# Kernel tuning notes

Measured on AMD Instinct MI355X. Metric: run time of the kernel, lower is better.

The kernel has to match this reference:

```python
import jax, jax.numpy as jnp
import numpy as np

BS, C, D = 4096, 16384, 128
POS_ALPHA, POS_DELTA = 32.0, 0.1
NEG_ALPHA, NEG_DELTA = 32.0, -0.1


def _normalize(x):
    # F.normalize(x, dim=1)
    return x / jnp.linalg.norm(x, axis=1, keepdims=True)


def _masked_lse(sims, mask, axis, use_max):
    """Faithful port of Criterion.masked_logsumexp (returns per-entry lse and the
    nonzero-entry mask that torch uses to filter before the final mean)."""
    m = sims * mask
    if use_max:
        ref = jnp.max(m, axis=axis, keepdims=True)
    else:
        ref = jnp.min(m, axis=axis, keepdims=True)
    ref = jax.lax.stop_gradient(ref)  # torch: ref_v.detach()
    # torch: nz_entries = max + min of (sims*mask); keep where nonzero
    nz = (jnp.max(m, axis=axis) + jnp.min(m, axis=axis)) != 0
    s = jnp.sum(jnp.exp(sims - ref) * mask, axis=axis)
    lse = jnp.log(jnp.where(nz, s, 1.0)) + jnp.squeeze(ref, axis=axis)
    return lse, nz


def setup_inputs() -> dict:
    key = jax.random.key(0)
    k1, k2, k3 = jax.random.split(key, 3)
    batch = jax.random.normal(k1, (BS, D), dtype=jnp.float32)
    # proxies = randn/proxy_div, init_dev=0 so no max-shift
    proxies = jax.random.normal(k2, (C, D), dtype=jnp.float32) / 8.0
    labels = jax.random.randint(k3, (BS,), 0, C)
    return {"batch": batch, "proxies": proxies, "labels": labels}


def reference(batch, proxies, labels):
    batch = _normalize(batch)          # [BS, D]
    proxies = _normalize(proxies)      # [C, D]

    pos_sims = batch @ proxies[labels].T   # [BS, BS] cosine sims to positive proxies
    sims = batch @ proxies.T               # [BS, C]

    same = (labels[:, None] == labels[None, :]).astype(batch.dtype)              # [BS, BS]
    diff = (labels[:, None] != jnp.arange(C)[None, :]).astype(batch.dtype)       # [BS, C]

    w_pos = -POS_ALPHA * (pos_sims - POS_DELTA)
    w_neg = NEG_ALPHA * (sims - NEG_DELTA)

    # mode='anchor' -> dim=0; cosine -> max=False for pos, max=True for neg
    pos_lse, pos_nz = _masked_lse(w_pos, same, axis=0, use_max=False)
    neg_lse, neg_nz = _masked_lse(w_neg, diff, axis=0, use_max=True)

    # nca_clean=False -> softplus
    pos_s = jax.nn.softplus(pos_lse)
    neg_s = jax.nn.softplus(neg_lse)

    # torch takes mean only over nz entries
    pos_mean = jnp.sum(jnp.where(pos_nz, pos_s, 0.0)) / jnp.maximum(jnp.sum(pos_nz), 1).astype(batch.dtype)
    neg_mean = jnp.sum(jnp.where(neg_nz, neg_s, 0.0)) / jnp.maximum(jnp.sum(neg_nz), 1).astype(batch.dtype)
    return pos_mean + neg_mean
```

## Files before the change

kernel.cpp:

```cpp
#include <hip/hip_runtime.h>
#include <math.h>

#define BS 4096
#define C_CLS 16384
#define D 128
#define NS 16
#define NR 4
#define KE 46.16624130844683f
#define POS_C 4.616624130844683f
#define LN2 0.69314718055994531f
#define CORR_BLOCKS 256
#define NEG_BLOCKS 2048

typedef __attribute__((ext_vector_type(8))) short short8;
typedef __attribute__((ext_vector_type(4))) float f32x4;

__device__ inline float bf2f(unsigned short h) {
    return __uint_as_float(((unsigned)h) << 16);
}
__device__ inline unsigned short f2bf(float f) {
    unsigned u = __float_as_uint(f);
    u += 0x7FFF + ((u >> 16) & 1);
    return (unsigned short)(u >> 16);
}
__device__ inline float fastexp2(float x) {
    return __int_as_float((int)fmaf(x, 8388608.0f, 1064866816.0f));
}
__device__ inline float softplus(float x) {
    return fmaxf(x, 0.0f) + log1pf(__expf(-fabsf(x)));
}
__device__ inline void gload16(const void* g, void* l) {
    __builtin_amdgcn_global_load_lds((const __attribute__((address_space(1))) void*)g,
                                     (__attribute__((address_space(3))) void*)l, 16, 0, 0);
}
__device__ inline unsigned fenc(float f) {
    unsigned u = __float_as_uint(f);
    return (u & 0x80000000u) ? ~u : (u | 0x80000000u);
}
__device__ inline float fdec(unsigned k) {
    return (k & 0x80000000u) ? __uint_as_float(k ^ 0x80000000u) : __uint_as_float(~k);
}

__global__ __launch_bounds__(256) void normalize_all(const float* __restrict__ batch,
                                                     const float* __restrict__ proxies,
                                                     short* __restrict__ bbf,
                                                     short* __restrict__ pbf,
                                                     float* __restrict__ acc,
                                                     float* __restrict__ negSub,
                                                     float* __restrict__ posSum,
                                                     float* __restrict__ posCnt,
                                                     unsigned* __restrict__ posMaxK,
                                                     unsigned* __restrict__ posMinK,
                                                     int* __restrict__ counter) {
    const int sub = threadIdx.x >> 5;
    const int lane32 = threadIdx.x & 31;
    const int row = blockIdx.x * 8 + sub;
    const bool isb = row < BS;
    const float* src = isb ? batch : proxies;
    short* dst = isb ? bbf : pbf;
    const int r = isb ? row : row - BS;
    const float sc = isb ? 1.0f : KE;

    float4 v = ((const float4*)(src + (size_t)r * D))[lane32];
    float ss = v.x * v.x + v.y * v.y + v.z * v.z + v.w * v.w;
#pragma unroll
    for (int off = 16; off; off >>= 1) ss += __shfl_xor(ss, off);
    float inv = rsqrtf(ss) * sc;
    ushort4 o;
    o.x = f2bf(v.x * inv);
    o.y = f2bf(v.y * inv);
    o.z = f2bf(v.z * inv);
    o.w = f2bf(v.w * inv);
    ((ushort4*)(dst + (size_t)r * D))[lane32] = o;

    const int bid = blockIdx.x, t = threadIdx.x;
    if (bid < 64) negSub[bid * 256 + t] = 0.0f;
    else if (bid < 128) posSum[(bid - 64) * 256 + t] = 0.0f;
    else if (bid < 192) posCnt[(bid - 128) * 256 + t] = 0.0f;
    else if (bid < 256) posMaxK[(bid - 192) * 256 + t] = 0u;
    else if (bid < 320) posMinK[(bid - 256) * 256 + t] = 0xFFFFFFFFu;
    if (bid == 0 && t == 0) *counter = 0;
}

__global__ __launch_bounds__(256, 1) void mm_all(const short* __restrict__ pbf,
                                                 const short* __restrict__ bbf,
                                                 const int* __restrict__ labels,
                                                 float* __restrict__ S,
                                                 float* __restrict__ negSub,
                                                 float* __restrict__ posSum,
                                                 float* __restrict__ posCnt,
                                                 unsigned* __restrict__ posMaxK,
                                                 unsigned* __restrict__ posMinK) {
    __shared__ short8 frag[2][16 * 64];

    const int bid = blockIdx.x;
    const int tid = threadIdx.x;
    const int w = tid >> 6, lane = tid & 63, l16 = lane & 15, g = lane >> 4;

    if (bid < CORR_BLOCKS) {
        const int ibase = bid * 16 + w * 4;
        int lab[4];
        float d[4];
#pragma unroll
        for (int r = 0; r < 4; r++) {
            const int i = ibase + r;
            lab[r] = labels[i];
            ushort2 av = ((const ushort2*)(bbf + (size_t)i * D))[lane];
            ushort2 pv = ((const ushort2*)(pbf + (size_t)lab[r] * D))[lane];
            d[r] = bf2f(av.x) * bf2f(pv.x) + bf2f(av.y) * bf2f(pv.y);
        }
#pragma unroll
        for (int off = 32; off; off >>= 1)
#pragma unroll
            for (int r = 0; r < 4; r++) d[r] += __shfl_xor(d[r], off);

        if (lane == 0) {
#pragma unroll
            for (int r = 0; r < 4; r++) {
                atomicAdd(&negSub[lab[r]], fastexp2(d[r]));
                atomicAdd(&posSum[lab[r]], fastexp2(POS_C - d[r]));
                atomicAdd(&posCnt[lab[r]], 1.0f);
                unsigned k = fenc(fmaf(d[r], -LN2, 3.2f));
                atomicMax(&posMaxK[lab[r]], k);
                atomicMin(&posMinK[lab[r]], k);
            }
        }
        return;
    }

    const int n = bid - CORR_BLOCKS;
    const int pg = (n & 7) * 16 + ((n >> 3) & 15);
    const int sp = n >> 7;
    const int wbase = pg * 128 + w * 32;

    short8 a[2][4];
#pragma unroll
    for (int pt = 0; pt < 2; pt++)
#pragma unroll
        for (int kk = 0; kk < 4; kk++)
            a[pt][kk] = *(const short8*)(pbf + (size_t)(wbase + pt * 16 + l16) * D + kk * 32 + g * 8);
#pragma unroll
    for (int pt = 0; pt < 2; pt++)
#pragma unroll
        for (int kk = 0; kk < 4; kk++)
            asm volatile("" : "+v"(a[pt][kk]));

    float s[2][4];
#pragma unroll
    for (int pt = 0; pt < 2; pt++)
#pragma unroll
        for (int r = 0; r < 4; r++) s[pt][r] = 0.0f;

    const int ibeg = sp * (BS / NS);
    const short* srcbase = bbf + (size_t)(ibeg + w * 16 + l16) * D + g * 8;

#define STAGE(rr)                                                            \
    {                                                                        \
        const short* sn_ = srcbase + (size_t)(rr) * 64 * D;                  \
        _Pragma("unroll") for (int kk = 0; kk < 4; kk++)                     \
            gload16(sn_ + kk * 32, &frag[(rr) & 1][(w * 4 + kk) * 64]);      \
    }

    STAGE(0)
    asm volatile("s_waitcnt vmcnt(0)" ::: "memory");
    __syncthreads();

    for (int rnd = 0; rnd < NR; rnd++) {
        const int cur = rnd & 1;
        if (rnd + 1 < NR) STAGE(rnd + 1)

        const short8* fb = &frag[cur][0];
#pragma unroll
        for (int bt = 0; bt < 4; bt++) {
            short8 b[4];
#pragma unroll
            for (int kk = 0; kk < 4; kk++) b[kk] = fb[(bt * 4 + kk) * 64 + lane];
#pragma unroll
            for (int pt = 0; pt < 2; pt++) {
                f32x4 acc = {0.0f, 0.0f, 0.0f, 0.0f};
#pragma unroll
                for (int kk = 0; kk < 4; kk++)
                    acc = __builtin_amdgcn_mfma_f32_16x16x32_bf16(a[pt][kk], b[kk], acc, 0, 0, 0);
#pragma unroll
                for (int r = 0; r < 4; r++) s[pt][r] += fastexp2(acc[r]);
            }
        }
        asm volatile("s_waitcnt vmcnt(0)" ::: "memory");
        __syncthreads();
    }
#undef STAGE

#pragma unroll
    for (int off = 1; off < 16; off <<= 1)
#pragma unroll
        for (int pt = 0; pt < 2; pt++)
#pragma unroll
            for (int r = 0; r < 4; r++) s[pt][r] += __shfl_xor(s[pt][r], off);

    if (l16 == 0) {
#pragma unroll
        for (int pt = 0; pt < 2; pt++)
#pragma unroll
            for (int r = 0; r < 4; r++) {
                int row = wbase + pt * 16 + g * 4 + r;
                S[(size_t)sp * C_CLS + row] = s[pt][r];
            }
    }
}

__global__ __launch_bounds__(256) void final_reduce(const float* __restrict__ S,
                                                    const float* __restrict__ negSub,
                                                    const int* __restrict__ labels,
                                                    const float* __restrict__ posSum,
                                                    const float* __restrict__ posCnt,
                                                    const unsigned* __restrict__ posMaxK,
                                                    const unsigned* __restrict__ posMinK,
                                                    float* __restrict__ acc,
                                                    int* __restrict__ counter,
                                                    float* __restrict__ out) {
    const int n = blockIdx.x * 256 + threadIdx.x;
    float add = 0.0f, cnt = 0.0f;
    int slot;
    if (n < C_CLS) {
        slot = 2;
        float s = 0.0f;
#pragma unroll
        for (int p = 0; p < NS; p++) s += S[(size_t)p * C_CLS + n];
        s = fmaxf(s - negSub[n], 1e-30f);
        add = softplus(logf(s) + 3.2f);
        cnt = 1.0f;
    } else {
        slot = 0;
        const int j = n - C_CLS;
        const int lab = labels[j];
        float s = posSum[lab], c = posCnt[lab];
        float mxw = fdec(posMaxK[lab]), mnw = fdec(posMinK[lab]);
        float maxm = (c < (float)BS) ? fmaxf(mxw, 0.0f) : mxw;
        float minm = (c < (float)BS) ? fminf(mnw, 0.0f) : mnw;
        bool nz = (maxm + minm) != 0.0f;
        if (nz) {
            add = softplus(logf(s));
            cnt = 1.0f;
        }
    }
#pragma unroll
    for (int off = 32; off; off >>= 1) {
        add += __shfl_xor(add, off);
        cnt += __shfl_xor(cnt, off);
    }
    if ((threadIdx.x & 63) == 0) {
        atomicAdd(&acc[slot], add);
        atomicAdd(&acc[slot + 1], cnt);
    }

    __shared__ int amLast;
    __threadfence();
    if (threadIdx.x == 0) amLast = (atomicAdd(counter, 1) == (int)gridDim.x - 1);
    __syncthreads();
    if (amLast && threadIdx.x == 0) {
        __threadfence();
        out[0] = acc[0] / fmaxf(acc[1], 1.0f) + acc[2] / fmaxf(acc[3], 1.0f);
    }
}

extern "C" void kernel_launch(void* const* d_in, const int* in_sizes, int n_in,
                              void* d_out, int out_size, void* d_ws, size_t ws_size,
                              hipStream_t stream) {
    const float* batch = (const float*)d_in[0];
    const float* proxies = (const float*)d_in[1];
    const int* labels = (const int*)d_in[2];
    float* out = (float*)d_out;

    char* ws = (char*)d_ws;
    float* acc = (float*)ws;
    int* counter = (int*)(ws + 64);
    short* bbf = (short*)(ws + 256);
    short* pbf = (short*)(ws + 256 + (size_t)BS * D * 2);
    char* p = ws + 256 + (size_t)(BS + C_CLS) * D * 2;
    float* negS = (float*)p;          p += (size_t)C_CLS * NS * 4;
    float* negSub = (float*)p;        p += (size_t)C_CLS * 4;
    float* posSum = (float*)p;        p += (size_t)C_CLS * 4;
    float* posCnt = (float*)p;        p += (size_t)C_CLS * 4;
    unsigned* posMaxK = (unsigned*)p; p += (size_t)C_CLS * 4;
    unsigned* posMinK = (unsigned*)p;

    normalize_all<<<(BS + C_CLS) / 8, 256, 0, stream>>>(batch, proxies, bbf, pbf, acc,
                                                        negSub, posSum, posCnt, posMaxK,
                                                        posMinK, counter);
    mm_all<<<CORR_BLOCKS + NEG_BLOCKS, 256, 0, stream>>>(pbf, bbf, labels, negS, negSub,
                                                         posSum, posCnt, posMaxK, posMinK);
    final_reduce<<<(C_CLS + BS) / 256, 256, 0, stream>>>(negS, negSub, labels, posSum,
                                                         posCnt, posMaxK, posMinK,
                                                         acc, counter, out);
}
```

Before: 49.90 us.

## Switch neg GEMM to 32x32x16 MFMA tiles with 64 proxies per wave

Replaces the 16x16x32 bf16 MFMA tiling with 32x32x16 MFMA, so each wave now covers 64 proxy rows instead of 32, and halves the number of neg blocks. The LDS staging layout, the A-fragment loads and the output row mapping are reworked to match the 32x32 operand layout, and the cross-lane reduction now spans 32 lanes. The aim is higher MFMA throughput and more reuse of each staged batch tile. In exchange it uses more registers (16-wide accumulators, 16 A fragments) and launches fewer blocks, which could hurt occupancy and load balance.

```diff
diff --git a/kernel.cpp b/kernel.cpp
--- a/kernel.cpp
+++ b/kernel.cpp
@@ -10,10 +10,10 @@
 #define POS_C 4.616624130844683f
 #define LN2 0.69314718055994531f
 #define CORR_BLOCKS 256
-#define NEG_BLOCKS 2048
+#define NEG_BLOCKS 1024
 
 typedef __attribute__((ext_vector_type(8))) short short8;
-typedef __attribute__((ext_vector_type(4))) float f32x4;
+typedef __attribute__((ext_vector_type(16))) float f32x16;
 
 __device__ inline float bf2f(unsigned short h) {
     return __uint_as_float(((unsigned)h) << 16);
@@ -95,7 +95,7 @@
 
     const int bid = blockIdx.x;
     const int tid = threadIdx.x;
-    const int w = tid >> 6, lane = tid & 63, l16 = lane & 15, g = lane >> 4;
+    const int w = tid >> 6, lane = tid & 63;
 
     if (bid < CORR_BLOCKS) {
         const int ibase = bid * 16 + w * 4;
@@ -128,37 +128,41 @@
         return;
     }
 
+    const int l32 = lane & 31, hi = lane >> 5;
     const int n = bid - CORR_BLOCKS;
-    const int pg = (n & 7) * 16 + ((n >> 3) & 15);
-    const int sp = n >> 7;
-    const int wbase = pg * 128 + w * 32;
-
-    short8 a[2][4];
+    const int pg = (n & 7) * 8 + ((n >> 3) & 7);
+    const int sp = n >> 6;
+    const int wbase = pg * 256 + w * 64;
+
+    short8 a[2][8];
 #pragma unroll
     for (int pt = 0; pt < 2; pt++)
 #pragma unroll
-        for (int kk = 0; kk < 4; kk++)
-            a[pt][kk] = *(const short8*)(pbf + (size_t)(wbase + pt * 16 + l16) * D + kk * 32 + g * 8);
+        for (int kk = 0; kk < 8; kk++)
+            a[pt][kk] = *(const short8*)(pbf + (size_t)(wbase + pt * 32 + l32) * D + kk * 16 + hi * 8);
 #pragma unroll
     for (int pt = 0; pt < 2; pt++)
 #pragma unroll
-        for (int kk = 0; kk < 4; kk++)
+        for (int kk = 0; kk < 8; kk++)
             asm volatile("" : "+v"(a[pt][kk]));
 
-    float s[2][4];
+    float s[2][16];
 #pragma unroll
     for (int pt = 0; pt < 2; pt++)
 #pragma unroll
-        for (int r = 0; r < 4; r++) s[pt][r] = 0.0f;
+        for (int r = 0; r < 16; r++) s[pt][r] = 0.0f;
 
     const int ibeg = sp * (BS / NS);
-    const short* srcbase = bbf + (size_t)(ibeg + w * 16 + l16) * D + g * 8;
-
-#define STAGE(rr)                                                            \
-    {                                                                        \
-        const short* sn_ = srcbase + (size_t)(rr) * 64 * D;                  \
-        _Pragma("unroll") for (int kk = 0; kk < 4; kk++)                     \
-            gload16(sn_ + kk * 32, &frag[(rr) & 1][(w * 4 + kk) * 64]);      \
+
+#define STAGE(rr)                                                                      \
+    {                                                                                  \
+        _Pragma("unroll") for (int jj = 0; jj < 4; jj++) {                             \
+            const int idx_ = w * 4 + jj;                                               \
+            const int cg_ = idx_ >> 3, kk_ = idx_ & 7;                                 \
+            const short* sn_ = bbf +                                                   \
+                (size_t)(ibeg + (rr) * 64 + cg_ * 32 + l32) * D + kk_ * 16 + hi * 8;   \
+            gload16(sn_, &frag[(rr) & 1][idx_ * 64]);                                  \
+        }                                                                              \
     }
 
     STAGE(0)
@@ -171,18 +175,18 @@
 
         const short8* fb = &frag[cur][0];
 #pragma unroll
-        for (int bt = 0; bt < 4; bt++) {
-            short8 b[4];
-#pragma unroll
-            for (int kk = 0; kk < 4; kk++) b[kk] = fb[(bt * 4 + kk) * 64 + lane];
+        for (int cg = 0; cg < 2; cg++) {
+            short8 b[8];
+#pragma unroll
+            for (int kk = 0; kk < 8; kk++) b[kk] = fb[(cg * 8 + kk) * 64 + lane];
 #pragma unroll
             for (int pt = 0; pt < 2; pt++) {
-                f32x4 acc = {0.0f, 0.0f, 0.0f, 0.0f};
-#pragma unroll
-                for (int kk = 0; kk < 4; kk++)
-                    acc = __builtin_amdgcn_mfma_f32_16x16x32_bf16(a[pt][kk], b[kk], acc, 0, 0, 0);
-#pragma unroll
-                for (int r = 0; r < 4; r++) s[pt][r] += fastexp2(acc[r]);
+                f32x16 acc = {0};
+#pragma unroll
+                for (int kk = 0; kk < 8; kk++)
+                    acc = __builtin_amdgcn_mfma_f32_32x32x16_bf16(a[pt][kk], b[kk], acc, 0, 0, 0);
+#pragma unroll
+                for (int r = 0; r < 16; r++) s[pt][r] += fastexp2(acc[r]);
             }
         }
         asm volatile("s_waitcnt vmcnt(0)" ::: "memory");
@@ -191,18 +195,18 @@
 #undef STAGE
 
 #pragma unroll
-    for (int off = 1; off < 16; off <<= 1)
+    for (int off = 1; off < 32; off <<= 1)
 #pragma unroll
         for (int pt = 0; pt < 2; pt++)
 #pragma unroll
-            for (int r = 0; r < 4; r++) s[pt][r] += __shfl_xor(s[pt][r], off);
-
-    if (l16 == 0) {
+            for (int r = 0; r < 16; r++) s[pt][r] += __shfl_xor(s[pt][r], off);
+
+    if (l32 == 0) {
 #pragma unroll
         for (int pt = 0; pt < 2; pt++)
 #pragma unroll
-            for (int r = 0; r < 4; r++) {
-                int row = wbase + pt * 16 + g * 4 + r;
+            for (int r = 0; r < 16; r++) {
+                int row = wbase + pt * 32 + (r & 3) + 8 * (r >> 2) + 4 * hi;
                 S[(size_t)sp * C_CLS + row] = s[pt][r];
             }
     }
```

New measurement: 61.31 us. +22.9%, slower.
